# Kernel optimization log

Hardware: AMD Instinct MI355X
Metric: run time of the kernel (lower is better)

The kernel has to match this reference:

```python
import jax, jax.numpy as jnp
import numpy as np

N = 50000      # nodes
E = 800000     # edges (avg degree 16)
D_IN = 128
D_OUT = 128


def setup_inputs() -> dict:
    key = jax.random.key(0)
    k = jax.random.split(key, 6)
    x = jax.random.normal(k[0], (N, D_IN), dtype=jnp.float32)
    rows = jax.random.randint(k[1], (E,), 0, N, dtype=jnp.int32)   # destination nodes
    cols = jax.random.randint(k[2], (E,), 0, N, dtype=jnp.int32)   # source nodes
    vals = jax.random.uniform(k[3], (E,), dtype=jnp.float32)       # adj edge weights
    W = jax.random.normal(k[4], (D_OUT, D_IN), dtype=jnp.float32) * (1.0 / np.sqrt(D_IN))
    b = jax.random.normal(k[5], (D_OUT,), dtype=jnp.float32) * 0.01
    return {"x": x, "rows": rows, "cols": cols, "vals": vals, "W": W, "b": b}


def reference(x, rows, cols, vals, W, b):
    # Linear: h = x @ W^T + b   (torch nn.Linear convention, W: [out, in])
    h = jnp.einsum("ni,oi->no", x, W) + b            # [N, D_OUT]
    # spmm(adj, h): out[i] = sum_{(i,j) in E} vals_ij * h[j]
    msgs = h[cols] * vals[:, None]                    # [E, D_OUT]
    out = jax.ops.segment_sum(msgs, rows, num_segments=N)  # [N, D_OUT]
    return out
```

## Files before the change

### kernel.cpp

```cpp
#include <hip/hip_runtime.h>

#define D 128
#define SCAN_BLK 256
#define SCAN_THREADS 1024

typedef short  bf16x8 __attribute__((ext_vector_type(8)));
typedef float  f32x4  __attribute__((ext_vector_type(4)));

static __device__ __forceinline__ unsigned short f2bf(float f) {
    unsigned u = __float_as_uint(f);
    u += 0x7FFFu + ((u >> 16) & 1u);
    return (unsigned short)(u >> 16);
}
static __device__ __forceinline__ float bf2f_lo(unsigned u) {
    return __uint_as_float((u & 0xFFFFu) << 16);
}
static __device__ __forceinline__ float bf2f_hi(unsigned u) {
    return __uint_as_float(u & 0xFFFF0000u);
}

__global__ __launch_bounds__(256) void fused_pre(
    const int* __restrict__ rows, int* __restrict__ counts, int n_edges,
    const float* __restrict__ W, unsigned short* __restrict__ Wb, int histBlocks) {
    int bid = blockIdx.x;
    if (bid < histBlocks) {
        int i = bid * 256 + threadIdx.x;
        if (i < n_edges) atomicAdd(&counts[rows[i]], 1);
    } else {
        int i = (bid - histBlocks) * 256 + threadIdx.x;
        if (i < D * D) Wb[i] = f2bf(W[i]);
    }
}

__global__ __launch_bounds__(256) void fused_main(
    const int* __restrict__ rows, const int* __restrict__ cols,
    const float* __restrict__ vals, int* __restrict__ cursor,
    int2* __restrict__ evec, int n_edges, int permSlots,
    const float* __restrict__ x, const unsigned short* __restrict__ Wb,
    const float* __restrict__ b, unsigned short* __restrict__ hb, int n_rows) {
    const int bid = blockIdx.x;
    const int g   = bid / 5;
    const int r5  = bid % 5;

    if (r5 >= 2) {
        const int slot   = g * 3 + (r5 - 2);
        const int stride = permSlots * 256;
        for (int i = slot * 256 + threadIdx.x; i < n_edges; i += stride) {
            int rr  = rows[i];
            int pos = atomicAdd(&cursor[rr], 1);
            evec[pos] = make_int2(cols[i], __float_as_int(vals[i]));
        }
        return;
    }

    const int gb   = g * 2 + r5;
    const int lane = threadIdx.x & 63;
    const int wv   = threadIdx.x >> 6;
    const int row0 = gb * 64 + wv * 16;
    if (row0 >= n_rows) return;
    const int m  = lane & 15;
    const int kg = lane >> 4;

    int arow = row0 + m;
    if (arow >= n_rows) arow = n_rows - 1;
    const float* xr = x + (size_t)arow * D + kg * 8;

    f32x4 acc[8];
#pragma unroll
    for (int n = 0; n < 8; ++n) acc[n] = (f32x4){0.f, 0.f, 0.f, 0.f};

#pragma unroll
    for (int ks = 0; ks < 4; ++ks) {
        float4 f0 = *(const float4*)(xr + ks * 32);
        float4 f1 = *(const float4*)(xr + ks * 32 + 4);
        bf16x8 a;
        a[0] = (short)f2bf(f0.x); a[1] = (short)f2bf(f0.y);
        a[2] = (short)f2bf(f0.z); a[3] = (short)f2bf(f0.w);
        a[4] = (short)f2bf(f1.x); a[5] = (short)f2bf(f1.y);
        a[6] = (short)f2bf(f1.z); a[7] = (short)f2bf(f1.w);
#pragma unroll
        for (int n = 0; n < 8; ++n) {
            bf16x8 bf = *(const bf16x8*)&Wb[(size_t)(n * 16 + m) * D + ks * 32 + kg * 8];
            acc[n] = __builtin_amdgcn_mfma_f32_16x16x32_bf16(a, bf, acc[n], 0, 0, 0);
        }
    }

#pragma unroll
    for (int n = 0; n < 8; ++n) {
        int col = n * 16 + m;
        float bc = b[col];
#pragma unroll
        for (int j = 0; j < 4; ++j) {
            int rr = row0 + kg * 4 + j;
            if (rr < n_rows) hb[(size_t)rr * D + col] = f2bf(acc[n][j] + bc);
        }
    }
}

__global__ __launch_bounds__(SCAN_BLK) void scan_local(
    const int* __restrict__ counts, int* __restrict__ offs,
    int* __restrict__ blockSums, int n) {
    __shared__ int sh[SCAN_BLK];
    const int t = threadIdx.x;
    const int i = blockIdx.x * SCAN_BLK + t;
    int v = (i < n) ? counts[i] : 0;
    sh[t] = v;
    __syncthreads();
    for (int off = 1; off < SCAN_BLK; off <<= 1) {
        int add = (t >= off) ? sh[t - off] : 0;
        __syncthreads();
        sh[t] += add;
        __syncthreads();
    }
    if (i < n) offs[i] = sh[t] - v;
    if (t == SCAN_BLK - 1) blockSums[blockIdx.x] = sh[SCAN_BLK - 1];
}

__global__ __launch_bounds__(1024) void scan_blocks(
    int* __restrict__ blockSums, int* __restrict__ total, int nb) {
    __shared__ int sh[1024];
    const int t = threadIdx.x;
    int v = (t < nb) ? blockSums[t] : 0;
    sh[t] = v;
    __syncthreads();
    for (int off = 1; off < 1024; off <<= 1) {
        int add = (t >= off) ? sh[t - off] : 0;
        __syncthreads();
        sh[t] += add;
        __syncthreads();
    }
    if (t < nb) blockSums[t] = sh[t] - v;
    if (t == 1023) *total = sh[1023];
}

__global__ __launch_bounds__(SCAN_BLK) void scan_add(
    int* __restrict__ offs, int* __restrict__ cursor,
    const int* __restrict__ blockSums, int n) {
    const int i = blockIdx.x * SCAN_BLK + threadIdx.x;
    if (i < n) {
        int o = offs[i] + blockSums[blockIdx.x];
        offs[i]   = o;
        cursor[i] = o;
    }
}

__global__ __launch_bounds__(SCAN_THREADS) void scan_counts(
    const int* __restrict__ counts, int* __restrict__ offs,
    int* __restrict__ cursor, int n) {
    __shared__ int part[SCAN_THREADS];
    const int t = threadIdx.x;
    const int chunk = (n + SCAN_THREADS - 1) / SCAN_THREADS;
    const int s = t * chunk;
    const int e = min(s + chunk, n);
    int sum = 0;
    for (int i = s; i < e; ++i) sum += counts[i];
    part[t] = sum;
    __syncthreads();
    for (int off = 1; off < SCAN_THREADS; off <<= 1) {
        int add = (t >= off) ? part[t - off] : 0;
        __syncthreads();
        part[t] += add;
        __syncthreads();
    }
    int run = part[t] - sum;
    for (int i = s; i < e; ++i) {
        offs[i]   = run;
        cursor[i] = run;
        run += counts[i];
    }
    if (e == n) offs[n] = run;
}

__global__ __launch_bounds__(256) void aggregate(
    const int* __restrict__ offs, const int2* __restrict__ evec,
    const unsigned short* __restrict__ hb, float* __restrict__ out, int n_nodes) {
    int wid = blockIdx.x * (blockDim.x >> 6) + (threadIdx.x >> 6);
    if (wid >= n_nodes) return;
    int lane = threadIdx.x & 63;

    int s = offs[wid];
    int e = offs[wid + 1];
    float2 acc = make_float2(0.f, 0.f);

    int k = s;
    if ((k & 1) && k < e) {
        int2 e0 = evec[k];
        unsigned u0 = *(const unsigned*)&hb[(size_t)e0.x * D + lane * 2];
        float v0 = __int_as_float(e0.y);
        acc.x += v0 * bf2f_lo(u0); acc.y += v0 * bf2f_hi(u0);
        ++k;
    }
    for (; k + 7 < e; k += 8) {
        int4 p0 = *(const int4*)&evec[k];
        int4 p1 = *(const int4*)&evec[k + 2];
        int4 p2 = *(const int4*)&evec[k + 4];
        int4 p3 = *(const int4*)&evec[k + 6];
        unsigned u0 = *(const unsigned*)&hb[(size_t)p0.x * D + lane * 2];
        unsigned u1 = *(const unsigned*)&hb[(size_t)p0.z * D + lane * 2];
        unsigned u2 = *(const unsigned*)&hb[(size_t)p1.x * D + lane * 2];
        unsigned u3 = *(const unsigned*)&hb[(size_t)p1.z * D + lane * 2];
        unsigned u4 = *(const unsigned*)&hb[(size_t)p2.x * D + lane * 2];
        unsigned u5 = *(const unsigned*)&hb[(size_t)p2.z * D + lane * 2];
        unsigned u6 = *(const unsigned*)&hb[(size_t)p3.x * D + lane * 2];
        unsigned u7 = *(const unsigned*)&hb[(size_t)p3.z * D + lane * 2];
        float v0 = __int_as_float(p0.y), v1 = __int_as_float(p0.w);
        float v2 = __int_as_float(p1.y), v3 = __int_as_float(p1.w);
        float v4 = __int_as_float(p2.y), v5 = __int_as_float(p2.w);
        float v6 = __int_as_float(p3.y), v7 = __int_as_float(p3.w);
        acc.x += v0 * bf2f_lo(u0); acc.y += v0 * bf2f_hi(u0);
        acc.x += v1 * bf2f_lo(u1); acc.y += v1 * bf2f_hi(u1);
        acc.x += v2 * bf2f_lo(u2); acc.y += v2 * bf2f_hi(u2);
        acc.x += v3 * bf2f_lo(u3); acc.y += v3 * bf2f_hi(u3);
        acc.x += v4 * bf2f_lo(u4); acc.y += v4 * bf2f_hi(u4);
        acc.x += v5 * bf2f_lo(u5); acc.y += v5 * bf2f_hi(u5);
        acc.x += v6 * bf2f_lo(u6); acc.y += v6 * bf2f_hi(u6);
        acc.x += v7 * bf2f_lo(u7); acc.y += v7 * bf2f_hi(u7);
    }
    for (; k + 1 < e; k += 2) {
        int4 p0 = *(const int4*)&evec[k];
        unsigned u0 = *(const unsigned*)&hb[(size_t)p0.x * D + lane * 2];
        unsigned u1 = *(const unsigned*)&hb[(size_t)p0.z * D + lane * 2];
        float v0 = __int_as_float(p0.y), v1 = __int_as_float(p0.w);
        acc.x += v0 * bf2f_lo(u0); acc.y += v0 * bf2f_hi(u0);
        acc.x += v1 * bf2f_lo(u1); acc.y += v1 * bf2f_hi(u1);
    }
    if (k < e) {
        int2 e0 = evec[k];
        unsigned u0 = *(const unsigned*)&hb[(size_t)e0.x * D + lane * 2];
        float v0 = __int_as_float(e0.y);
        acc.x += v0 * bf2f_lo(u0); acc.y += v0 * bf2f_hi(u0);
    }

    *(float2*)&out[(size_t)wid * D + lane * 2] = acc;
}

__global__ __launch_bounds__(256) void scatter_add(
    const int* __restrict__ rows, const int* __restrict__ cols,
    const float* __restrict__ vals, const unsigned short* __restrict__ hb,
    float* __restrict__ out, int n_edges) {
    long long gid = (long long)blockIdx.x * blockDim.x + threadIdx.x;
    int e  = (int)(gid >> 5);
    if (e >= n_edges) return;
    int d4 = ((int)gid & 31) * 4;
    int   r = rows[e];
    int   c = cols[e];
    float v = vals[e];
    const unsigned short* hp = &hb[(size_t)c * D + d4];
    unsigned u0 = *(const unsigned*)(hp + 0);
    unsigned u1 = *(const unsigned*)(hp + 2);
    float* op = &out[(size_t)r * D + d4];
    atomicAdd(op + 0, v * bf2f_lo(u0));
    atomicAdd(op + 1, v * bf2f_hi(u0));
    atomicAdd(op + 2, v * bf2f_lo(u1));
    atomicAdd(op + 3, v * bf2f_hi(u1));
}

__global__ void convert_W(const float* __restrict__ W, unsigned short* __restrict__ Wb) {
    int i = blockIdx.x * blockDim.x + threadIdx.x;
    if (i < D * D) Wb[i] = f2bf(W[i]);
}

__global__ __launch_bounds__(256) void gemm_mfma(
    const float* __restrict__ x, const unsigned short* __restrict__ Wb,
    const float* __restrict__ b, unsigned short* __restrict__ hb, int n_rows) {
    const int lane = threadIdx.x & 63;
    const int wv   = threadIdx.x >> 6;
    const int row0 = blockIdx.x * 64 + wv * 16;
    if (row0 >= n_rows) return;
    const int m  = lane & 15;
    const int kg = lane >> 4;
    int arow = row0 + m;
    if (arow >= n_rows) arow = n_rows - 1;
    const float* xr = x + (size_t)arow * D + kg * 8;
    f32x4 acc[8];
#pragma unroll
    for (int n = 0; n < 8; ++n) acc[n] = (f32x4){0.f, 0.f, 0.f, 0.f};
#pragma unroll
    for (int ks = 0; ks < 4; ++ks) {
        float4 f0 = *(const float4*)(xr + ks * 32);
        float4 f1 = *(const float4*)(xr + ks * 32 + 4);
        bf16x8 a;
        a[0] = (short)f2bf(f0.x); a[1] = (short)f2bf(f0.y);
        a[2] = (short)f2bf(f0.z); a[3] = (short)f2bf(f0.w);
        a[4] = (short)f2bf(f1.x); a[5] = (short)f2bf(f1.y);
        a[6] = (short)f2bf(f1.z); a[7] = (short)f2bf(f1.w);
#pragma unroll
        for (int n = 0; n < 8; ++n) {
            bf16x8 bf = *(const bf16x8*)&Wb[(size_t)(n * 16 + m) * D + ks * 32 + kg * 8];
            acc[n] = __builtin_amdgcn_mfma_f32_16x16x32_bf16(a, bf, acc[n], 0, 0, 0);
        }
    }
#pragma unroll
    for (int n = 0; n < 8; ++n) {
        int col = n * 16 + m;
        float bc = b[col];
#pragma unroll
        for (int j = 0; j < 4; ++j) {
            int r = row0 + kg * 4 + j;
            if (r < n_rows) hb[(size_t)r * D + col] = f2bf(acc[n][j] + bc);
        }
    }
}

static inline size_t align16(size_t x) { return (x + 15) & ~(size_t)15; }

extern "C" void kernel_launch(void* const* d_in, const int* in_sizes, int n_in,
                              void* d_out, int out_size, void* d_ws, size_t ws_size,
                              hipStream_t stream) {
    const float* x    = (const float*)d_in[0];
    const int*   rows = (const int*)  d_in[1];
    const int*   cols = (const int*)  d_in[2];
    const float* vals = (const float*)d_in[3];
    const float* W    = (const float*)d_in[4];
    const float* b    = (const float*)d_in[5];
    float*       out  = (float*)d_out;

    const int n_nodes = in_sizes[0] / D;
    const int n_edges = in_sizes[1];
    const int nScanBlocks = (n_nodes + SCAN_BLK - 1) / SCAN_BLK;
    const int histBlocks  = (n_edges + 255) / 256;
    const int convBlocks  = (D * D + 255) / 256;
    const int gemmBlocks  = (n_nodes + 63) / 64;
    const int nGroups     = (gemmBlocks + 1) / 2;
    const int permSlots   = nGroups * 3;
    const int mainBlocks  = nGroups * 5;

    char*  base    = (char*)d_ws;
    size_t off     = 0;
    unsigned short* Wb = (unsigned short*)(base + off); off = align16(off + (size_t)D * D * 2);
    unsigned short* hb = (unsigned short*)(base + off); off = align16(off + (size_t)n_nodes * D * 2);
    int*   counts  = (int*)  (base + off); off = align16(off + (size_t)n_nodes * 4);
    int*   offs    = (int*)  (base + off); off = align16(off + ((size_t)n_nodes + 1) * 4);
    int*   cursor  = (int*)  (base + off); off = align16(off + (size_t)n_nodes * 4);
    int*   bsums   = (int*)  (base + off); off = align16(off + (size_t)1024 * 4);
    int2*  evec    = (int2*) (base + off); off = align16(off + (size_t)n_edges * 8);
    const bool csr_fits = (off <= ws_size);

    if (csr_fits) {
        hipMemsetAsync(counts, 0, (size_t)n_nodes * 4, stream);
        fused_pre<<<histBlocks + convBlocks, 256, 0, stream>>>(
            rows, counts, n_edges, W, Wb, histBlocks);
        if (nScanBlocks <= 1024) {
            scan_local<<<nScanBlocks, SCAN_BLK, 0, stream>>>(counts, offs, bsums, n_nodes);
            scan_blocks<<<1, 1024, 0, stream>>>(bsums, &offs[n_nodes], nScanBlocks);
            scan_add<<<nScanBlocks, SCAN_BLK, 0, stream>>>(offs, cursor, bsums, n_nodes);
        } else {
            scan_counts<<<1, SCAN_THREADS, 0, stream>>>(counts, offs, cursor, n_nodes);
        }
        fused_main<<<mainBlocks, 256, 0, stream>>>(
            rows, cols, vals, cursor, evec, n_edges, permSlots,
            x, Wb, b, hb, n_nodes);
        aggregate<<<(n_nodes + 3) / 4, 256, 0, stream>>>(offs, evec, hb, out, n_nodes);
    } else {
        convert_W<<<convBlocks, 256, 0, stream>>>(W, Wb);
        gemm_mfma<<<gemmBlocks, 256, 0, stream>>>(x, Wb, b, hb, n_nodes);
        hipMemsetAsync(d_out, 0, (size_t)n_nodes * D * sizeof(float), stream);
        long long scatter_threads = (long long)n_edges * 32;
        int scatter_blocks = (int)((scatter_threads + 255) / 256);
        scatter_add<<<scatter_blocks, 256, 0, stream>>>(rows, cols, vals, hb, out, n_edges);
    }
}
```

Measured before the change: 141.4 us.

## Store edge indices instead of col/val pairs in CSR permutation

The permutation step now writes only the original edge index (4 bytes) per edge instead of a (col, val) pair. The aggregate kernel then gathers cols and vals through that index. This reduces scattered write traffic in the permute phase but adds an extra dependent random gather per edge in aggregation. The GEMM part also preloads all x fragments before converting to bf16, and launch bounds hint 4 blocks per CU.

```diff
diff --git a/kernel.cpp b/kernel.cpp
--- a/kernel.cpp
+++ b/kernel.cpp
@@ -32,10 +32,9 @@
     }
 }
 
-__global__ __launch_bounds__(256) void fused_main(
-    const int* __restrict__ rows, const int* __restrict__ cols,
-    const float* __restrict__ vals, int* __restrict__ cursor,
-    int2* __restrict__ evec, int n_edges, int permSlots,
+__global__ __launch_bounds__(256, 4) void fused_main(
+    const int* __restrict__ rows, int* __restrict__ cursor,
+    int* __restrict__ eidx, int n_edges, int permSlots,
     const float* __restrict__ x, const unsigned short* __restrict__ Wb,
     const float* __restrict__ b, unsigned short* __restrict__ hb, int n_rows) {
     const int bid = blockIdx.x;
@@ -48,7 +47,7 @@
         for (int i = slot * 256 + threadIdx.x; i < n_edges; i += stride) {
             int rr  = rows[i];
             int pos = atomicAdd(&cursor[rr], 1);
-            evec[pos] = make_int2(cols[i], __float_as_int(vals[i]));
+            eidx[pos] = i;
         }
         return;
     }
@@ -65,23 +64,34 @@
     if (arow >= n_rows) arow = n_rows - 1;
     const float* xr = x + (size_t)arow * D + kg * 8;
 
-    f32x4 acc[8];
-#pragma unroll
-    for (int n = 0; n < 8; ++n) acc[n] = (f32x4){0.f, 0.f, 0.f, 0.f};
-
+    float4 xf[8];
 #pragma unroll
     for (int ks = 0; ks < 4; ++ks) {
-        float4 f0 = *(const float4*)(xr + ks * 32);
-        float4 f1 = *(const float4*)(xr + ks * 32 + 4);
+        xf[2 * ks]     = *(const float4*)(xr + ks * 32);
+        xf[2 * ks + 1] = *(const float4*)(xr + ks * 32 + 4);
+    }
+    bf16x8 afr[4];
+#pragma unroll
+    for (int ks = 0; ks < 4; ++ks) {
+        float4 f0 = xf[2 * ks], f1 = xf[2 * ks + 1];
         bf16x8 a;
         a[0] = (short)f2bf(f0.x); a[1] = (short)f2bf(f0.y);
         a[2] = (short)f2bf(f0.z); a[3] = (short)f2bf(f0.w);
         a[4] = (short)f2bf(f1.x); a[5] = (short)f2bf(f1.y);
         a[6] = (short)f2bf(f1.z); a[7] = (short)f2bf(f1.w);
+        afr[ks] = a;
+    }
+
+    f32x4 acc[8];
+#pragma unroll
+    for (int n = 0; n < 8; ++n) acc[n] = (f32x4){0.f, 0.f, 0.f, 0.f};
+
+#pragma unroll
+    for (int ks = 0; ks < 4; ++ks) {
 #pragma unroll
         for (int n = 0; n < 8; ++n) {
             bf16x8 bf = *(const bf16x8*)&Wb[(size_t)(n * 16 + m) * D + ks * 32 + kg * 8];
-            acc[n] = __builtin_amdgcn_mfma_f32_16x16x32_bf16(a, bf, acc[n], 0, 0, 0);
+            acc[n] = __builtin_amdgcn_mfma_f32_16x16x32_bf16(afr[ks], bf, acc[n], 0, 0, 0);
         }
     }
 
@@ -171,42 +181,43 @@
     if (e == n) offs[n] = run;
 }
 
-__global__ __launch_bounds__(256) void aggregate(
-    const int* __restrict__ offs, const int2* __restrict__ evec,
+__global__ __launch_bounds__(256, 4) void aggregate(
+    const int* __restrict__ offs, const int* __restrict__ eidx,
+    const int* __restrict__ cols, const float* __restrict__ vals,
     const unsigned short* __restrict__ hb, float* __restrict__ out, int n_nodes) {
-    int wid = blockIdx.x * (blockDim.x >> 6) + (threadIdx.x >> 6);
+    int wid = blockIdx.x * 4 + (threadIdx.x >> 6);
     if (wid >= n_nodes) return;
     int lane = threadIdx.x & 63;
 
-    int s = offs[wid];
-    int e = offs[wid + 1];
+    const int s = offs[wid];
+    const int e = offs[wid + 1];
+    const int c0 = lane * 2;
     float2 acc = make_float2(0.f, 0.f);
 
     int k = s;
-    if ((k & 1) && k < e) {
-        int2 e0 = evec[k];
-        unsigned u0 = *(const unsigned*)&hb[(size_t)e0.x * D + lane * 2];
-        float v0 = __int_as_float(e0.y);
-        acc.x += v0 * bf2f_lo(u0); acc.y += v0 * bf2f_hi(u0);
+    while ((k & 3) && k < e) {
+        int   eid = eidx[k];
+        int   c   = cols[eid];
+        float v   = vals[eid];
+        unsigned u = *(const unsigned*)&hb[(size_t)c * D + c0];
+        acc.x += v * bf2f_lo(u); acc.y += v * bf2f_hi(u);
         ++k;
     }
     for (; k + 7 < e; k += 8) {
-        int4 p0 = *(const int4*)&evec[k];
-        int4 p1 = *(const int4*)&evec[k + 2];
-        int4 p2 = *(const int4*)&evec[k + 4];
-        int4 p3 = *(const int4*)&evec[k + 6];
-        unsigned u0 = *(const unsigned*)&hb[(size_t)p0.x * D + lane * 2];
-        unsigned u1 = *(const unsigned*)&hb[(size_t)p0.z * D + lane * 2];
-        unsigned u2 = *(const unsigned*)&hb[(size_t)p1.x * D + lane * 2];
-        unsigned u3 = *(const unsigned*)&hb[(size_t)p1.z * D + lane * 2];
-        unsigned u4 = *(const unsigned*)&hb[(size_t)p2.x * D + lane * 2];
-        unsigned u5 = *(const unsigned*)&hb[(size_t)p2.z * D + lane * 2];
-        unsigned u6 = *(const unsigned*)&hb[(size_t)p3.x * D + lane * 2];
-        unsigned u7 = *(const unsigned*)&hb[(size_t)p3.z * D + lane * 2];
-        float v0 = __int_as_float(p0.y), v1 = __int_as_float(p0.w);
-        float v2 = __int_as_float(p1.y), v3 = __int_as_float(p1.w);
-        float v4 = __int_as_float(p2.y), v5 = __int_as_float(p2.w);
-        float v6 = __int_as_float(p3.y), v7 = __int_as_float(p3.w);
+        int4 a0 = *(const int4*)&eidx[k];
+        int4 a1 = *(const int4*)&eidx[k + 4];
+        int ci0 = cols[a0.x], ci1 = cols[a0.y], ci2 = cols[a0.z], ci3 = cols[a0.w];
+        int ci4 = cols[a1.x], ci5 = cols[a1.y], ci6 = cols[a1.z], ci7 = cols[a1.w];
+        float v0 = vals[a0.x], v1 = vals[a0.y], v2 = vals[a0.z], v3 = vals[a0.w];
+        float v4 = vals[a1.x], v5 = vals[a1.y], v6 = vals[a1.z], v7 = vals[a1.w];
+        unsigned u0 = *(const unsigned*)&hb[(size_t)ci0 * D + c0];
+        unsigned u1 = *(const unsigned*)&hb[(size_t)ci1 * D + c0];
+        unsigned u2 = *(const unsigned*)&hb[(size_t)ci2 * D + c0];
+        unsigned u3 = *(const unsigned*)&hb[(size_t)ci3 * D + c0];
+        unsigned u4 = *(const unsigned*)&hb[(size_t)ci4 * D + c0];
+        unsigned u5 = *(const unsigned*)&hb[(size_t)ci5 * D + c0];
+        unsigned u6 = *(const unsigned*)&hb[(size_t)ci6 * D + c0];
+        unsigned u7 = *(const unsigned*)&hb[(size_t)ci7 * D + c0];
         acc.x += v0 * bf2f_lo(u0); acc.y += v0 * bf2f_hi(u0);
         acc.x += v1 * bf2f_lo(u1); acc.y += v1 * bf2f_hi(u1);
         acc.x += v2 * bf2f_lo(u2); acc.y += v2 * bf2f_hi(u2);
@@ -216,22 +227,62 @@
         acc.x += v6 * bf2f_lo(u6); acc.y += v6 * bf2f_hi(u6);
         acc.x += v7 * bf2f_lo(u7); acc.y += v7 * bf2f_hi(u7);
     }
-    for (; k + 1 < e; k += 2) {
-        int4 p0 = *(const int4*)&evec[k];
-        unsigned u0 = *(const unsigned*)&hb[(size_t)p0.x * D + lane * 2];
-        unsigned u1 = *(const unsigned*)&hb[(size_t)p0.z * D + lane * 2];
-        float v0 = __int_as_float(p0.y), v1 = __int_as_float(p0.w);
-        acc.x += v0 * bf2f_lo(u0); acc.y += v0 * bf2f_hi(u0);
-        acc.x += v1 * bf2f_lo(u1); acc.y += v1 * bf2f_hi(u1);
-    }
-    if (k < e) {
-        int2 e0 = evec[k];
-        unsigned u0 = *(const unsigned*)&hb[(size_t)e0.x * D + lane * 2];
-        float v0 = __int_as_float(e0.y);
-        acc.x += v0 * bf2f_lo(u0); acc.y += v0 * bf2f_hi(u0);
-    }
-
-    *(float2*)&out[(size_t)wid * D + lane * 2] = acc;
+    for (; k < e; ++k) {
+        int   eid = eidx[k];
+        int   c   = cols[eid];
+        float v   = vals[eid];
+        unsigned u = *(const unsigned*)&hb[(size_t)c * D + c0];
+        acc.x += v * bf2f_lo(u); acc.y += v * bf2f_hi(u);
+    }
+
+    *(float2*)&out[(size_t)wid * D + c0] = acc;
+}
+
+__global__ void convert_W(const float* __restrict__ W, unsigned short* __restrict__ Wb) {
+    int i = blockIdx.x * blockDim.x + threadIdx.x;
+    if (i < D * D) Wb[i] = f2bf(W[i]);
+}
+
+__global__ __launch_bounds__(256) void gemm_mfma(
+    const float* __restrict__ x, const unsigned short* __restrict__ Wb,
+    const float* __restrict__ b, unsigned short* __restrict__ hb, int n_rows) {
+    const int lane = threadIdx.x & 63;
+    const int wv   = threadIdx.x >> 6;
+    const int row0 = blockIdx.x * 64 + wv * 16;
+    if (row0 >= n_rows) return;
+    const int m  = lane & 15;
+    const int kg = lane >> 4;
+    int arow = row0 + m;
+    if (arow >= n_rows) arow = n_rows - 1;
+    const float* xr = x + (size_t)arow * D + kg * 8;
+    f32x4 acc[8];
+#pragma unroll
+    for (int n = 0; n < 8; ++n) acc[n] = (f32x4){0.f, 0.f, 0.f, 0.f};
+#pragma unroll
+    for (int ks = 0; ks < 4; ++ks) {
+        float4 f0 = *(const float4*)(xr + ks * 32);
+        float4 f1 = *(const float4*)(xr + ks * 32 + 4);
+        bf16x8 a;
+        a[0] = (short)f2bf(f0.x); a[1] = (short)f2bf(f0.y);
+        a[2] = (short)f2bf(f0.z); a[3] = (short)f2bf(f0.w);
+        a[4] = (short)f2bf(f1.x); a[5] = (short)f2bf(f1.y);
+        a[6] = (short)f2bf(f1.z); a[7] = (short)f2bf(f1.w);
+#pragma unroll
+        for (int n = 0; n < 8; ++n) {
+            bf16x8 bf = *(const bf16x8*)&Wb[(size_t)(n * 16 + m) * D + ks * 32 + kg * 8];
+            acc[n] = __builtin_amdgcn_mfma_f32_16x16x32_bf16(a, bf, acc[n], 0, 0, 0);
+        }
+    }
+#pragma unroll
+    for (int n = 0; n < 8; ++n) {
+        int col = n * 16 + m;
+        float bc = b[col];
+#pragma unroll
+        for (int j = 0; j < 4; ++j) {
+            int r = row0 + kg * 4 + j;
+            if (r < n_rows) hb[(size_t)r * D + col] = f2bf(acc[n][j] + bc);
+        }
+    }
 }
 
 __global__ __launch_bounds__(256) void scatter_add(
@@ -255,53 +306,6 @@
     atomicAdd(op + 3, v * bf2f_hi(u1));
 }
 
-__global__ void convert_W(const float* __restrict__ W, unsigned short* __restrict__ Wb) {
-    int i = blockIdx.x * blockDim.x + threadIdx.x;
-    if (i < D * D) Wb[i] = f2bf(W[i]);
-}
-
-__global__ __launch_bounds__(256) void gemm_mfma(
-    const float* __restrict__ x, const unsigned short* __restrict__ Wb,
-    const float* __restrict__ b, unsigned short* __restrict__ hb, int n_rows) {
-    const int lane = threadIdx.x & 63;
-    const int wv   = threadIdx.x >> 6;
-    const int row0 = blockIdx.x * 64 + wv * 16;
-    if (row0 >= n_rows) return;
-    const int m  = lane & 15;
-    const int kg = lane >> 4;
-    int arow = row0 + m;
-    if (arow >= n_rows) arow = n_rows - 1;
-    const float* xr = x + (size_t)arow * D + kg * 8;
-    f32x4 acc[8];
-#pragma unroll
-    for (int n = 0; n < 8; ++n) acc[n] = (f32x4){0.f, 0.f, 0.f, 0.f};
-#pragma unroll
-    for (int ks = 0; ks < 4; ++ks) {
-        float4 f0 = *(const float4*)(xr + ks * 32);
-        float4 f1 = *(const float4*)(xr + ks * 32 + 4);
-        bf16x8 a;
-        a[0] = (short)f2bf(f0.x); a[1] = (short)f2bf(f0.y);
-        a[2] = (short)f2bf(f0.z); a[3] = (short)f2bf(f0.w);
-        a[4] = (short)f2bf(f1.x); a[5] = (short)f2bf(f1.y);
-        a[6] = (short)f2bf(f1.z); a[7] = (short)f2bf(f1.w);
-#pragma unroll
-        for (int n = 0; n < 8; ++n) {
-            bf16x8 bf = *(const bf16x8*)&Wb[(size_t)(n * 16 + m) * D + ks * 32 + kg * 8];
-            acc[n] = __builtin_amdgcn_mfma_f32_16x16x32_bf16(a, bf, acc[n], 0, 0, 0);
-        }
-    }
-#pragma unroll
-    for (int n = 0; n < 8; ++n) {
-        int col = n * 16 + m;
-        float bc = b[col];
-#pragma unroll
-        for (int j = 0; j < 4; ++j) {
-            int r = row0 + kg * 4 + j;
-            if (r < n_rows) hb[(size_t)r * D + col] = f2bf(acc[n][j] + bc);
-        }
-    }
-}
-
 static inline size_t align16(size_t x) { return (x + 15) & ~(size_t)15; }
 
 extern "C" void kernel_launch(void* const* d_in, const int* in_sizes, int n_in,
@@ -333,7 +337,7 @@
     int*   offs    = (int*)  (base + off); off = align16(off + ((size_t)n_nodes + 1) * 4);
     int*   cursor  = (int*)  (base + off); off = align16(off + (size_t)n_nodes * 4);
     int*   bsums   = (int*)  (base + off); off = align16(off + (size_t)1024 * 4);
-    int2*  evec    = (int2*) (base + off); off = align16(off + (size_t)n_edges * 8);
+    int*   eidx    = (int*)  (base + off); off = align16(off + (size_t)n_edges * 4);
     const bool csr_fits = (off <= ws_size);
 
     if (csr_fits) {
@@ -348,9 +352,10 @@
             scan_counts<<<1, SCAN_THREADS, 0, stream>>>(counts, offs, cursor, n_nodes);
         }
         fused_main<<<mainBlocks, 256, 0, stream>>>(
-            rows, cols, vals, cursor, evec, n_edges, permSlots,
+            rows, cursor, eidx, n_edges, permSlots,
             x, Wb, b, hb, n_nodes);
-        aggregate<<<(n_nodes + 3) / 4, 256, 0, stream>>>(offs, evec, hb, out, n_nodes);
+        aggregate<<<(n_nodes + 3) / 4, 256, 0, stream>>>(
+            offs, eidx, cols, vals, hb, out, n_nodes);
     } else {
         convert_W<<<convBlocks, 256, 0, stream>>>(W, Wb);
         gemm_mfma<<<gemmBlocks, 256, 0, stream>>>(x, Wb, b, hb, n_nodes);
```

Result: slower. 172.6 us (+22.1%).
